# Performance work log

Measured on AMD Instinct MI355X. Metric: run time of the kernel, lower is better.

The kernel has to match this reference:

```python
import jax, jax.numpy as jnp
import numpy as np

B, S, D = 32, 2048, 1024

def setup_inputs() -> dict:
    key = jax.random.key(0)
    k1, k2, k3, k4, k5, k6 = jax.random.split(key, 6)
    stdv = 1.0 / np.sqrt(D)
    return {
        "hidden": jax.random.normal(k1, (B, D), dtype=jnp.float32),
        "encoder_outputs": jax.random.normal(k2, (B, S, D), dtype=jnp.float32),
        "W": jax.random.normal(k3, (2 * D, D), dtype=jnp.float32) * stdv,  # linear_out weight (x @ W)
        "b": jax.random.normal(k4, (D,), dtype=jnp.float32) * stdv,
        "v": jax.random.normal(k5, (D,), dtype=jnp.float32) * stdv,
        "src_len": jax.random.randint(k6, (B,), 1, S + 1),
    }

def reference(hidden, encoder_outputs, W, b, v, src_len):
    # hidden: [B, D]; encoder_outputs: [B, S, D]
    Bb, Ss, Dd = encoder_outputs.shape
    H = jnp.broadcast_to(hidden[:, None, :], (Bb, Ss, Dd))      # repeat over seq
    x = jnp.concatenate([H, encoder_outputs], axis=-1)           # [B, S, 2D]
    energy = jnp.tanh(x @ W + b)                                 # [B, S, D]
    scores = jnp.einsum("bsd,d->bs", energy, v)                # v . energy
    mask = jnp.arange(Ss)[None, :] >= src_len[:, None]           # True = padding
    scores = jnp.where(mask, jnp.float32(-1e18), scores)
    attn = jax.nn.softmax(scores, axis=-1)                       # [B, S]
    return attn[:, None, :]                                      # [B, 1, S]
```

## Files before the change

kernel.cpp:

```cpp
#include <hip/hip_runtime.h>
#include <stdint.h>

#define B_ 32
#define S_ 2048
#define D_ 1024

typedef __bf16 bf16x8 __attribute__((ext_vector_type(8)));
typedef float f32x4 __attribute__((ext_vector_type(4)));

__device__ __forceinline__ void gload_lds16(const void* g, void* l) {
  __builtin_amdgcn_global_load_lds(
      (const __attribute__((address_space(1))) void*)g,
      (__attribute__((address_space(3))) void*)l, 16, 0, 0);
}

__global__ void zero_scores_k(float4* p) {
  p[blockIdx.x * 256 + threadIdx.x] = make_float4(0.f, 0.f, 0.f, 0.f);
}

__global__ __launch_bounds__(256) void conv_w2_k(const float* __restrict__ W,
                                                 unsigned short* __restrict__ W2t) {
  __shared__ float t[64][65];
  int k0 = blockIdx.x * 64, n0 = blockIdx.y * 64;
  int tx = threadIdx.x & 63, ty = threadIdx.x >> 6;
#pragma unroll
  for (int i = 0; i < 16; ++i) {
    int k = i * 4 + ty;
    t[k][tx] = W[(size_t)(D_ + k0 + k) * D_ + n0 + tx];
  }
  __syncthreads();
#pragma unroll
  for (int i = 0; i < 16; ++i) {
    int n = i * 4 + ty;
    __bf16 bv = (__bf16)t[tx][n];
    W2t[(size_t)(n0 + n) * D_ + k0 + tx] = *(unsigned short*)&bv;
  }
}

__global__ __launch_bounds__(256) void compute_u_k(const float* __restrict__ hidden,
                                                   const float* __restrict__ W,
                                                   const float* __restrict__ bias,
                                                   float* __restrict__ u) {
  __shared__ float h[D_];
  int b = blockIdx.x, nc = blockIdx.y;
  for (int i = threadIdx.x; i < D_; i += 256) h[i] = hidden[b * D_ + i];
  __syncthreads();
  int n = nc * 256 + threadIdx.x;
  float acc = bias[n];
#pragma unroll 8
  for (int k = 0; k < D_; ++k) acc = fmaf(h[k], W[(size_t)k * D_ + n], acc);
  u[b * D_ + n] = acc;
}

__global__ __launch_bounds__(256) void bahdanau_gemm_k(
    const float* __restrict__ enc, const unsigned short* __restrict__ W2t,
    const float* __restrict__ u, const float* __restrict__ vvec,
    const int* __restrict__ src_len, float* __restrict__ scores) {
  __shared__ __align__(16) unsigned short As[2][4096];
  __shared__ __align__(16) unsigned short Bs[2][4096];

  int bid = blockIdx.x;
  int mlow = bid & 7;
  int rem = bid >> 3;
  int nb = rem & 7;
  int mt = (rem >> 3) * 8 + mlow;
  int m0 = mt << 7;
  int n0 = nb << 7;
  int b = m0 >> 11;
  int s0 = m0 & (S_ - 1);
  if (s0 >= src_len[b]) return;

  int tid = threadIdx.x;
  int lane = tid & 63;
  int w = tid >> 6;
  int wm = (w >> 1) << 6;
  int wn = (w & 1) << 6;

  int arow = tid >> 1, ahalf = tid & 1;
  const float* aptr = enc + (size_t)(m0 + arow) * D_ + ahalf * 16;
  int ac0 = ((ahalf << 1) | 0) ^ (arow & 3);
  int ac1 = ((ahalf << 1) | 1) ^ (arow & 3);

  int seg0 = w << 1;
  int bn0 = (seg0 << 4) + (lane >> 2);
  int bn1 = bn0 + 16;
  int bc = (lane & 3) ^ (bn0 & 3);
  const unsigned short* bsrc0 = W2t + (size_t)(n0 + bn0) * D_ + bc * 8;
  const unsigned short* bsrc1 = W2t + (size_t)(n0 + bn1) * D_ + bc * 8;

  int lrow = lane & 15, lkc = lane >> 4;
  int fragoff = (wm + lrow) * 64 + ((lkc ^ (lrow & 3)) << 4);
  int fragoffB = (wn + lrow) * 64 + ((lkc ^ (lrow & 3)) << 4);

  float4 ar[4];
  f32x4 acc[4][4];
  f32x4 zero = {0.f, 0.f, 0.f, 0.f};
#pragma unroll
  for (int i = 0; i < 4; ++i)
#pragma unroll
    for (int j = 0; j < 4; ++j) acc[i][j] = zero;

  {
    const float4* p = (const float4*)aptr;
    ar[0] = p[0]; ar[1] = p[1]; ar[2] = p[2]; ar[3] = p[3];
    gload_lds16(bsrc0, &Bs[0][seg0 << 9]);
    gload_lds16(bsrc1, &Bs[0][(seg0 + 1) << 9]);
    bf16x8 w0, w1;
    const float* f = (const float*)ar;
#pragma unroll
    for (int j = 0; j < 8; ++j) { w0[j] = (__bf16)f[j]; w1[j] = (__bf16)f[8 + j]; }
    *(bf16x8*)((char*)As[0] + arow * 64 + (ac0 << 4)) = w0;
    *(bf16x8*)((char*)As[0] + arow * 64 + (ac1 << 4)) = w1;
  }
  __syncthreads();

  int buf = 0;
  for (int kt = 0; kt < 32; ++kt) {
    if (kt < 31) {
      const float4* p = (const float4*)(aptr + (kt + 1) * 32);
      ar[0] = p[0]; ar[1] = p[1]; ar[2] = p[2]; ar[3] = p[3];
      gload_lds16(bsrc0 + (kt + 1) * 32, &Bs[buf ^ 1][seg0 << 9]);
      gload_lds16(bsrc1 + (kt + 1) * 32, &Bs[buf ^ 1][(seg0 + 1) << 9]);
    }
    const char* ab = (const char*)As[buf] + fragoff;
    const char* bb = (const char*)Bs[buf] + fragoffB;
    bf16x8 af[4], bfr[4];
#pragma unroll
    for (int i = 0; i < 4; ++i) af[i] = *(const bf16x8*)(ab + i * 1024);
#pragma unroll
    for (int i = 0; i < 4; ++i) bfr[i] = *(const bf16x8*)(bb + i * 1024);
#pragma unroll
    for (int i = 0; i < 4; ++i)
#pragma unroll
      for (int j = 0; j < 4; ++j)
        acc[i][j] = __builtin_amdgcn_mfma_f32_16x16x32_bf16(af[i], bfr[j], acc[i][j], 0, 0, 0);
    if (kt < 31) {
      bf16x8 w0, w1;
      const float* f = (const float*)ar;
#pragma unroll
      for (int j = 0; j < 8; ++j) { w0[j] = (__bf16)f[j]; w1[j] = (__bf16)f[8 + j]; }
      *(bf16x8*)((char*)As[buf ^ 1] + arow * 64 + (ac0 << 4)) = w0;
      *(bf16x8*)((char*)As[buf ^ 1] + arow * 64 + (ac1 << 4)) = w1;
    }
    __syncthreads();
    buf ^= 1;
  }

  float uv[4], vv[4];
#pragma unroll
  for (int j = 0; j < 4; ++j) {
    int n = n0 + wn + j * 16 + lrow;
    uv[j] = u[(b << 10) + n];
    vv[j] = vvec[n];
  }
  float part[4][4];
#pragma unroll
  for (int i = 0; i < 4; ++i)
#pragma unroll
    for (int r = 0; r < 4; ++r) part[i][r] = 0.f;
#pragma unroll
  for (int i = 0; i < 4; ++i)
#pragma unroll
    for (int j = 0; j < 4; ++j)
#pragma unroll
      for (int r = 0; r < 4; ++r) {
        float z = acc[i][j][r] + uv[j];
        float e2 = __expf(2.0f * z);
        float th = 1.0f - 2.0f * __builtin_amdgcn_rcpf(e2 + 1.0f);
        part[i][r] = fmaf(vv[j], th, part[i][r]);
      }
#pragma unroll
  for (int i = 0; i < 4; ++i)
#pragma unroll
    for (int r = 0; r < 4; ++r) {
      float s = part[i][r];
      s += __shfl_xor(s, 1, 64);
      s += __shfl_xor(s, 2, 64);
      s += __shfl_xor(s, 4, 64);
      s += __shfl_xor(s, 8, 64);
      if ((lane & 15) == 0) {
        int row = s0 + wm + i * 16 + ((lane >> 4) << 2) + r;
        atomicAdd(&scores[(b << 11) + row], s);
      }
    }
}

__global__ __launch_bounds__(256) void softmax_k(const float* __restrict__ scores,
                                                 const int* __restrict__ src_len,
                                                 float* __restrict__ out) {
  __shared__ float sc[S_];
  __shared__ float red[4];
  int b = blockIdx.x;
  int L = src_len[b];
  int tid = threadIdx.x;
  const float* row = scores + b * S_;
  float mx = -3.0e38f;
  for (int s = tid; s < S_; s += 256) {
    float val = (s < L) ? row[s] : -3.0e38f;
    sc[s] = val;
    mx = fmaxf(mx, val);
  }
#pragma unroll
  for (int off = 32; off >= 1; off >>= 1) mx = fmaxf(mx, __shfl_xor(mx, off, 64));
  if ((tid & 63) == 0) red[tid >> 6] = mx;
  __syncthreads();
  mx = fmaxf(fmaxf(red[0], red[1]), fmaxf(red[2], red[3]));
  __syncthreads();
  float sum = 0.f;
  for (int s = tid; s < S_; s += 256) {
    float e = (s < L) ? __expf(sc[s] - mx) : 0.f;
    sc[s] = e;
    sum += e;
  }
#pragma unroll
  for (int off = 32; off >= 1; off >>= 1) sum += __shfl_xor(sum, off, 64);
  if ((tid & 63) == 0) red[tid >> 6] = sum;
  __syncthreads();
  sum = red[0] + red[1] + red[2] + red[3];
  float inv = 1.0f / sum;
  for (int s = tid; s < S_; s += 256) out[b * S_ + s] = sc[s] * inv;
}

extern "C" void kernel_launch(void* const* d_in, const int* in_sizes, int n_in,
                              void* d_out, int out_size, void* d_ws, size_t ws_size,
                              hipStream_t stream) {
  const float* hidden = (const float*)d_in[0];
  const float* enc = (const float*)d_in[1];
  const float* W = (const float*)d_in[2];
  const float* bias = (const float*)d_in[3];
  const float* v = (const float*)d_in[4];
  const int* src_len = (const int*)d_in[5];
  float* out = (float*)d_out;

  char* ws = (char*)d_ws;
  float* scores = (float*)ws;
  float* u = (float*)(ws + 256 * 1024);
  unsigned short* W2t = (unsigned short*)(ws + 384 * 1024);

  zero_scores_k<<<dim3(64), dim3(256), 0, stream>>>((float4*)scores);
  conv_w2_k<<<dim3(16, 16), dim3(256), 0, stream>>>(W, W2t);
  compute_u_k<<<dim3(32, 4), dim3(256), 0, stream>>>(hidden, W, bias, u);
  bahdanau_gemm_k<<<dim3(4096), dim3(256), 0, stream>>>(enc, W2t, u, v, src_len, scores);
  softmax_k<<<dim3(32), dim3(256), 0, stream>>>(scores, src_len, out);
}
```

Baseline: 607.9 us.

## Pre-convert encoder outputs to bf16 and stream both GEMM operands via direct LDS loads

Adds a separate pass that converts the valid encoder rows to bf16 in workspace. A new GEMM kernel then loads both operands with global_load_lds into single-buffered, unswizzled LDS tiles of 64-wide K, so the main loop no longer does fp32 loads and in-kernel conversion. The u projection is also split over K with atomic accumulation to expose more parallelism, and the zeroing kernel now clears u as well. The cost is an extra full read and write of the encoder tensor plus bank conflicts and lost overlap from dropping double buffering and swizzling; the old kernel remains as a fallback when workspace is too small.

```diff
diff --git a/kernel.cpp b/kernel.cpp
--- a/kernel.cpp
+++ b/kernel.cpp
@@ -14,7 +14,7 @@
       (__attribute__((address_space(3))) void*)l, 16, 0, 0);
 }
 
-__global__ void zero_scores_k(float4* p) {
+__global__ void zero_ws_k(float4* p) {
   p[blockIdx.x * 256 + threadIdx.x] = make_float4(0.f, 0.f, 0.f, 0.f);
 }
 
@@ -37,27 +37,49 @@
   }
 }
 
+__global__ __launch_bounds__(256) void conv_enc_k(const float* __restrict__ enc,
+                                                  unsigned short* __restrict__ encb,
+                                                  const int* __restrict__ src_len) {
+  int b = blockIdx.x, c = blockIdx.y;
+  int s0 = c * 32;
+  if (s0 >= src_len[b]) return;
+  size_t base = ((size_t)b * S_ + s0) * D_;
+  const float4* src = (const float4*)(enc + base);
+  bf16x8* dst = (bf16x8*)(encb + base);
+#pragma unroll 4
+  for (int i = threadIdx.x; i < 4096; i += 256) {
+    float4 a = src[2 * i], bq = src[2 * i + 1];
+    bf16x8 o;
+    o[0] = (__bf16)a.x;  o[1] = (__bf16)a.y;  o[2] = (__bf16)a.z;  o[3] = (__bf16)a.w;
+    o[4] = (__bf16)bq.x; o[5] = (__bf16)bq.y; o[6] = (__bf16)bq.z; o[7] = (__bf16)bq.w;
+    dst[i] = o;
+  }
+}
+
 __global__ __launch_bounds__(256) void compute_u_k(const float* __restrict__ hidden,
                                                    const float* __restrict__ W,
                                                    const float* __restrict__ bias,
                                                    float* __restrict__ u) {
-  __shared__ float h[D_];
-  int b = blockIdx.x, nc = blockIdx.y;
-  for (int i = threadIdx.x; i < D_; i += 256) h[i] = hidden[b * D_ + i];
-  __syncthreads();
-  int n = nc * 256 + threadIdx.x;
-  float acc = bias[n];
+  __shared__ float h[256];
+  int b = blockIdx.x, nc = blockIdx.y, kc = blockIdx.z;
+  int tid = threadIdx.x;
+  h[tid] = hidden[b * D_ + kc * 256 + tid];
+  __syncthreads();
+  int n = nc * 256 + tid;
+  float acc = 0.f;
 #pragma unroll 8
-  for (int k = 0; k < D_; ++k) acc = fmaf(h[k], W[(size_t)k * D_ + n], acc);
-  u[b * D_ + n] = acc;
-}
-
-__global__ __launch_bounds__(256) void bahdanau_gemm_k(
-    const float* __restrict__ enc, const unsigned short* __restrict__ W2t,
+  for (int k = 0; k < 256; ++k)
+    acc = fmaf(h[k], W[(size_t)(kc * 256 + k) * D_ + n], acc);
+  if (kc == 0) acc += bias[n];
+  atomicAdd(&u[b * D_ + n], acc);
+}
+
+__global__ __launch_bounds__(256) void bahdanau_gemm2_k(
+    const unsigned short* __restrict__ encb, const unsigned short* __restrict__ W2t,
     const float* __restrict__ u, const float* __restrict__ vvec,
     const int* __restrict__ src_len, float* __restrict__ scores) {
-  __shared__ __align__(16) unsigned short As[2][4096];
-  __shared__ __align__(16) unsigned short Bs[2][4096];
+  __shared__ __align__(16) unsigned short As[128 * 64];
+  __shared__ __align__(16) unsigned short Bs[128 * 64];
 
   int bid = blockIdx.x;
   int mlow = bid & 7;
@@ -76,22 +98,118 @@
   int wm = (w >> 1) << 6;
   int wn = (w & 1) << 6;
 
+  int srow = w * 32 + (lane >> 3);
+  int scol = (lane & 7) * 8;
+  const unsigned short* asrc = encb + (size_t)(m0 + srow) * D_ + scol;
+  const unsigned short* bsrc = W2t + (size_t)(n0 + srow) * D_ + scol;
+
+  int lrow = lane & 15, lkc = lane >> 4;
+
+  f32x4 acc[4][4];
+  f32x4 zero = {0.f, 0.f, 0.f, 0.f};
+#pragma unroll
+  for (int i = 0; i < 4; ++i)
+#pragma unroll
+    for (int j = 0; j < 4; ++j) acc[i][j] = zero;
+
+  for (int kt = 0; kt < 16; ++kt) {
+    __syncthreads();
+#pragma unroll
+    for (int q = 0; q < 4; ++q) {
+      gload_lds16(asrc + kt * 64 + (size_t)q * 8 * D_, As + (w * 32 + q * 8) * 64);
+      gload_lds16(bsrc + kt * 64 + (size_t)q * 8 * D_, Bs + (w * 32 + q * 8) * 64);
+    }
+    __syncthreads();
+#pragma unroll
+    for (int ks = 0; ks < 2; ++ks) {
+      bf16x8 af[4], bfr[4];
+#pragma unroll
+      for (int i = 0; i < 4; ++i)
+        af[i] = *(const bf16x8*)(As + (wm + i * 16 + lrow) * 64 + ks * 32 + lkc * 8);
+#pragma unroll
+      for (int j = 0; j < 4; ++j)
+        bfr[j] = *(const bf16x8*)(Bs + (wn + j * 16 + lrow) * 64 + ks * 32 + lkc * 8);
+#pragma unroll
+      for (int i = 0; i < 4; ++i)
+#pragma unroll
+        for (int j = 0; j < 4; ++j)
+          acc[i][j] = __builtin_amdgcn_mfma_f32_16x16x32_bf16(af[i], bfr[j], acc[i][j], 0, 0, 0);
+    }
+  }
+
+  float uv[4], vv[4];
+#pragma unroll
+  for (int j = 0; j < 4; ++j) {
+    int n = n0 + wn + j * 16 + lrow;
+    uv[j] = u[(b << 10) + n];
+    vv[j] = vvec[n];
+  }
+  float part[4][4];
+#pragma unroll
+  for (int i = 0; i < 4; ++i)
+#pragma unroll
+    for (int r = 0; r < 4; ++r) part[i][r] = 0.f;
+#pragma unroll
+  for (int i = 0; i < 4; ++i)
+#pragma unroll
+    for (int j = 0; j < 4; ++j)
+#pragma unroll
+      for (int r = 0; r < 4; ++r) {
+        float z = acc[i][j][r] + uv[j];
+        float e2 = __expf(2.0f * z);
+        float th = 1.0f - 2.0f * __builtin_amdgcn_rcpf(e2 + 1.0f);
+        part[i][r] = fmaf(vv[j], th, part[i][r]);
+      }
+#pragma unroll
+  for (int i = 0; i < 4; ++i)
+#pragma unroll
+    for (int r = 0; r < 4; ++r) {
+      float s = part[i][r];
+      s += __shfl_xor(s, 1, 64);
+      s += __shfl_xor(s, 2, 64);
+      s += __shfl_xor(s, 4, 64);
+      s += __shfl_xor(s, 8, 64);
+      if ((lane & 15) == 0) {
+        int row = s0 + wm + i * 16 + ((lane >> 4) << 2) + r;
+        atomicAdd(&scores[(b << 11) + row], s);
+      }
+    }
+}
+
+__global__ __launch_bounds__(256) void bahdanau_gemm_k(
+    const float* __restrict__ enc, const unsigned short* __restrict__ W2t,
+    const float* __restrict__ u, const float* __restrict__ vvec,
+    const int* __restrict__ src_len, float* __restrict__ scores) {
+  __shared__ __align__(16) unsigned short As[2][4096];
+  __shared__ __align__(16) unsigned short Bs[2][4096];
+  int bid = blockIdx.x;
+  int mlow = bid & 7;
+  int rem = bid >> 3;
+  int nb = rem & 7;
+  int mt = (rem >> 3) * 8 + mlow;
+  int m0 = mt << 7;
+  int n0 = nb << 7;
+  int b = m0 >> 11;
+  int s0 = m0 & (S_ - 1);
+  if (s0 >= src_len[b]) return;
+  int tid = threadIdx.x;
+  int lane = tid & 63;
+  int w = tid >> 6;
+  int wm = (w >> 1) << 6;
+  int wn = (w & 1) << 6;
   int arow = tid >> 1, ahalf = tid & 1;
   const float* aptr = enc + (size_t)(m0 + arow) * D_ + ahalf * 16;
   int ac0 = ((ahalf << 1) | 0) ^ (arow & 3);
   int ac1 = ((ahalf << 1) | 1) ^ (arow & 3);
-
   int seg0 = w << 1;
   int bn0 = (seg0 << 4) + (lane >> 2);
   int bn1 = bn0 + 16;
   int bc = (lane & 3) ^ (bn0 & 3);
   const unsigned short* bsrc0 = W2t + (size_t)(n0 + bn0) * D_ + bc * 8;
   const unsigned short* bsrc1 = W2t + (size_t)(n0 + bn1) * D_ + bc * 8;
-
   int lrow = lane & 15, lkc = lane >> 4;
   int fragoff = (wm + lrow) * 64 + ((lkc ^ (lrow & 3)) << 4);
   int fragoffB = (wn + lrow) * 64 + ((lkc ^ (lrow & 3)) << 4);
-
   float4 ar[4];
   f32x4 acc[4][4];
   f32x4 zero = {0.f, 0.f, 0.f, 0.f};
@@ -99,7 +217,6 @@
   for (int i = 0; i < 4; ++i)
 #pragma unroll
     for (int j = 0; j < 4; ++j) acc[i][j] = zero;
-
   {
     const float4* p = (const float4*)aptr;
     ar[0] = p[0]; ar[1] = p[1]; ar[2] = p[2]; ar[3] = p[3];
@@ -113,7 +230,6 @@
     *(bf16x8*)((char*)As[0] + arow * 64 + (ac1 << 4)) = w1;
   }
   __syncthreads();
-
   int buf = 0;
   for (int kt = 0; kt < 32; ++kt) {
     if (kt < 31) {
@@ -145,7 +261,6 @@
     __syncthreads();
     buf ^= 1;
   }
-
   float uv[4], vv[4];
 #pragma unroll
   for (int j = 0; j < 4; ++j) {
@@ -236,10 +351,17 @@
   float* scores = (float*)ws;
   float* u = (float*)(ws + 256 * 1024);
   unsigned short* W2t = (unsigned short*)(ws + 384 * 1024);
-
-  zero_scores_k<<<dim3(64), dim3(256), 0, stream>>>((float4*)scores);
+  unsigned short* encb = (unsigned short*)(ws + 4ull * 1024 * 1024);
+  const size_t need = 4ull * 1024 * 1024 + (size_t)B_ * S_ * D_ * 2;
+
+  zero_ws_k<<<dim3(96), dim3(256), 0, stream>>>((float4*)scores);
   conv_w2_k<<<dim3(16, 16), dim3(256), 0, stream>>>(W, W2t);
-  compute_u_k<<<dim3(32, 4), dim3(256), 0, stream>>>(hidden, W, bias, u);
-  bahdanau_gemm_k<<<dim3(4096), dim3(256), 0, stream>>>(enc, W2t, u, v, src_len, scores);
+  compute_u_k<<<dim3(32, 4, 4), dim3(256), 0, stream>>>(hidden, W, bias, u);
+  if (ws_size >= need) {
+    conv_enc_k<<<dim3(32, 64), dim3(256), 0, stream>>>(enc, encb, src_len);
+    bahdanau_gemm2_k<<<dim3(4096), dim3(256), 0, stream>>>(encb, W2t, u, v, src_len, scores);
+  } else {
+    bahdanau_gemm_k<<<dim3(4096), dim3(256), 0, stream>>>(enc, W2t, u, v, src_len, scores);
+  }
   softmax_k<<<dim3(32), dim3(256), 0, stream>>>(scores, src_len, out);
 }
```

Result: faster. 519.6 us (-14.5%).
